# Performance work log

Hardware: AMD Instinct MI355X
Metric: run time of the kernel (lower is better)

## Reference

```python
import jax, jax.numpy as jnp
import numpy as np

H = 64  # hidden_dim

def _rnn_layer(x, Wih, Whh, bih, bhh):
    # x: [B, T, D_in] -> hidden states [B, T, H]; PyTorch RNN tanh cell:
    # h_t = tanh(W_ih x_t + b_ih + W_hh h_{t-1} + b_hh)
    B = x.shape[0]
    xp = jnp.einsum('btd,hd->bth', x, Wih) + bih  # precompute input projection
    h0 = jnp.zeros((B, H), dtype=x.dtype)
    def step(h, xt):
        h = jnp.tanh(xt + h @ Whh.T + bhh)
        return h, h
    _, hs = jax.lax.scan(step, h0, jnp.swapaxes(xp, 0, 1))  # scan over T
    return jnp.swapaxes(hs, 0, 1)  # [B, T, H]

def setup_inputs() -> dict:
    key = jax.random.key(0)
    ks = jax.random.split(key, 14)
    B, T, D = 4096, 512, 1
    s = 0.1  # small init scale to keep tanh unsaturated
    inp = {
        'x': jax.random.normal(ks[0], (B, T, D), dtype=jnp.float32),
        'W_ih0': jax.random.normal(ks[1], (H, D), dtype=jnp.float32) * s,
        'W_hh0': jax.random.normal(ks[2], (H, H), dtype=jnp.float32) * s,
        'b_ih0': jax.random.normal(ks[3], (H,), dtype=jnp.float32) * s,
        'b_hh0': jax.random.normal(ks[4], (H,), dtype=jnp.float32) * s,
        'W_ih1': jax.random.normal(ks[5], (H, H), dtype=jnp.float32) * s,
        'W_hh1': jax.random.normal(ks[6], (H, H), dtype=jnp.float32) * s,
        'b_ih1': jax.random.normal(ks[7], (H,), dtype=jnp.float32) * s,
        'b_hh1': jax.random.normal(ks[8], (H,), dtype=jnp.float32) * s,
        'fc1_W': jax.random.normal(ks[9], (64, H), dtype=jnp.float32) * s,
        'fc1_b': jax.random.normal(ks[10], (64,), dtype=jnp.float32) * s,
        'fc2_W': jax.random.normal(ks[11], (1, 64), dtype=jnp.float32) * s,
        'fc2_b': jax.random.normal(ks[12], (1,), dtype=jnp.float32) * s,
    }
    return inp

def reference(x, W_ih0, W_hh0, b_ih0, b_hh0, W_ih1, W_hh1, b_ih1, b_hh1,
              fc1_W, fc1_b, fc2_W, fc2_b):
    h1 = _rnn_layer(x, W_ih0, W_hh0, b_ih0, b_hh0)   # layer 0
    h2 = _rnn_layer(h1, W_ih1, W_hh1, b_ih1, b_hh1)  # layer 1
    last = h2[:, -1, :]                               # [B, H]
    z = jax.nn.relu(last @ fc1_W.T + fc1_b)
    return z @ fc2_W.T + fc2_b                        # [B, 1]
```

## Files before the change

kernel.cpp:

```cpp
#include <hip/hip_runtime.h>

namespace {

constexpr int T_LEN = 512;
constexpr int XS    = 516;

typedef _Float16 half8  __attribute__((ext_vector_type(8)));
typedef float    f32x4v __attribute__((ext_vector_type(4)));
typedef unsigned uint2v __attribute__((ext_vector_type(2)));
typedef unsigned uint4v __attribute__((ext_vector_type(4)));

#define MFMA16(a, b, c) __builtin_amdgcn_mfma_f32_16x16x32_f16((a), (b), (c), 0, 0, 0)

__device__ __forceinline__ half8 load_frag(const float* __restrict__ W,
                                           int row, int k0, float s) {
    const float* p = W + row * 64 + k0;
    f32x4v lo = *reinterpret_cast<const f32x4v*>(p);
    f32x4v hi = *reinterpret_cast<const f32x4v*>(p + 4);
    uint4v u;
    u.x = __builtin_bit_cast(unsigned, __builtin_amdgcn_cvt_pkrtz(lo.x * s, lo.y * s));
    u.y = __builtin_bit_cast(unsigned, __builtin_amdgcn_cvt_pkrtz(lo.z * s, lo.w * s));
    u.z = __builtin_bit_cast(unsigned, __builtin_amdgcn_cvt_pkrtz(hi.x * s, hi.y * s));
    u.w = __builtin_bit_cast(unsigned, __builtin_amdgcn_cvt_pkrtz(hi.z * s, hi.w * s));
    return __builtin_bit_cast(half8, u);
}

__device__ __forceinline__ void tanh4(f32x4v &a) {
#pragma unroll
    for (int q = 0; q < 4; ++q) {
        float e = __expf(a[q]);
        a[q] = 1.0f - 2.0f * __builtin_amdgcn_rcpf(e + 1.0f);
    }
}

__global__ __launch_bounds__(256, 2)
void rnn_mfma4_kernel(const float* __restrict__ x,
                      const float* __restrict__ Wih0,
                      const float* __restrict__ Whh0,
                      const float* __restrict__ bih0,
                      const float* __restrict__ bhh0,
                      const float* __restrict__ Wih1,
                      const float* __restrict__ Whh1,
                      const float* __restrict__ bih1,
                      const float* __restrict__ bhh1,
                      const float* __restrict__ fc1W,
                      const float* __restrict__ fc1b,
                      const float* __restrict__ fc2W,
                      const float* __restrict__ fc2b,
                      float* __restrict__ out)
{
    const int tid    = threadIdx.x;
    const int wv     = tid >> 6;
    const int lane   = tid & 63;
    const int g      = lane >> 4;
    const int b16    = lane & 15;
    const int batch0 = blockIdx.x * 16;

    __shared__ float    sx[16 * XS];
    __shared__ _Float16 sh1[2][16][72];
    __shared__ _Float16 sh2[2][16][72];
    __shared__ float    pf[4][16];

    {
        const float* gx = x + (size_t)batch0 * T_LEN;
#pragma unroll
        for (int c = 0; c < 8; ++c) {
            int idx = tid + c * 256;
            int r = idx >> 7, c4 = idx & 127;
            f32x4v v = *reinterpret_cast<const f32x4v*>(gx + r * T_LEN + c4 * 4);
            *reinterpret_cast<f32x4v*>(&sx[r * XS + c4 * 4]) = v;
        }
    }

    const int row = 16 * wv + b16;
    const half8 WA0_0 = load_frag(Whh0, row,      8 * g, 2.0f);
    const half8 WA0_1 = load_frag(Whh0, row, 32 + 8 * g, 2.0f);
    const half8 WI1_0 = load_frag(Wih1, row,      8 * g, 2.0f);
    const half8 WI1_1 = load_frag(Wih1, row, 32 + 8 * g, 2.0f);
    const half8 WH1_0 = load_frag(Whh1, row,      8 * g, 2.0f);
    const half8 WH1_1 = load_frag(Whh1, row, 32 + 8 * g, 2.0f);

    f32x4v bb0, bb1, wx2;
#pragma unroll
    for (int q = 0; q < 4; ++q) {
        const int o = 16 * wv + 4 * g + q;
        bb0[q] = 2.0f * (bih0[o] + bhh0[o]);
        bb1[q] = 2.0f * (bih1[o] + bhh1[o]);
        wx2[q] = 2.0f * Wih0[o];
    }
    const int o2 = 16 * wv + 4 * g;

    auto publish = [&](_Float16* base, const f32x4v& a) {
        uint2v p;
        p.x = __builtin_bit_cast(unsigned, __builtin_amdgcn_cvt_pkrtz(a[0], a[1]));
        p.y = __builtin_bit_cast(unsigned, __builtin_amdgcn_cvt_pkrtz(a[2], a[3]));
        *reinterpret_cast<uint2v*>(base + b16 * 72 + o2) = p;
    };
    auto rdfrag = [&](const _Float16* base, int k0) -> half8 {
        return *reinterpret_cast<const half8*>(base + b16 * 72 + k0);
    };

    half8 Bh1_0, Bh1_1, Bh2_0, Bh2_1;

    __syncthreads();

    float xt = sx[b16 * XS + 0];
    float xn = sx[b16 * XS + 1];

    {
        f32x4v a0 = wx2 * xt + bb0;
        tanh4(a0);
        publish(&sh1[0][0][0], a0);
        *reinterpret_cast<uint2v*>(&sh2[0][0][0] + b16 * 72 + o2) = uint2v{0, 0};
        __syncthreads();
        Bh1_0 = rdfrag(&sh1[0][0][0],      8 * g);
        Bh1_1 = rdfrag(&sh1[0][0][0], 32 + 8 * g);
        Bh2_0 = rdfrag(&sh2[0][0][0],      8 * g);
        Bh2_1 = rdfrag(&sh2[0][0][0], 32 + 8 * g);
        xt = xn; xn = sx[b16 * XS + 2];
    }

#pragma unroll 2
    for (int k = 1; k < T_LEN; ++k) {
        const int s = k & 1;
        const float xf = sx[b16 * XS + k + 2];

        f32x4v a0 = wx2 * xt + bb0;
        a0 = MFMA16(WA0_0, Bh1_0, a0);
        a0 = MFMA16(WA0_1, Bh1_1, a0);

        f32x4v zz = {};
        f32x4v u  = MFMA16(WI1_0, Bh1_0, bb1);
        u  = MFMA16(WI1_1, Bh1_1, u);
        f32x4v v4 = MFMA16(WH1_0, Bh2_0, zz);
        v4 = MFMA16(WH1_1, Bh2_1, v4);
        f32x4v a1 = u + v4;

        tanh4(a0);
        tanh4(a1);
        publish(&sh1[s][0][0], a0);
        publish(&sh2[s][0][0], a1);
        __syncthreads();
        Bh1_0 = rdfrag(&sh1[s][0][0],      8 * g);
        Bh1_1 = rdfrag(&sh1[s][0][0], 32 + 8 * g);
        Bh2_0 = rdfrag(&sh2[s][0][0],      8 * g);
        Bh2_1 = rdfrag(&sh2[s][0][0], 32 + 8 * g);
        xt = xn; xn = xf;
    }

    {
        f32x4v zz = {};
        f32x4v u  = MFMA16(WI1_0, Bh1_0, bb1);
        u  = MFMA16(WI1_1, Bh1_1, u);
        f32x4v v4 = MFMA16(WH1_0, Bh2_0, zz);
        v4 = MFMA16(WH1_1, Bh2_1, v4);
        f32x4v a1 = u + v4;
        tanh4(a1);
        publish(&sh2[0][0][0], a1);
        __syncthreads();
        Bh2_0 = rdfrag(&sh2[0][0][0],      8 * g);
        Bh2_1 = rdfrag(&sh2[0][0][0], 32 + 8 * g);
    }

    const half8 F0 = load_frag(fc1W, row,      8 * g, 1.0f);
    const half8 F1 = load_frag(fc1W, row, 32 + 8 * g, 1.0f);
    f32x4v zf;
#pragma unroll
    for (int q = 0; q < 4; ++q) zf[q] = fc1b[16 * wv + 4 * g + q];
    zf = MFMA16(F0, Bh2_0, zf);
    zf = MFMA16(F1, Bh2_1, zf);

    float pacc = 0.0f;
#pragma unroll
    for (int q = 0; q < 4; ++q)
        pacc += fmaxf(zf[q], 0.0f) * fc2W[16 * wv + 4 * g + q];
    pacc += __shfl_xor(pacc, 16);
    pacc += __shfl_xor(pacc, 32);
    if (lane < 16) pf[wv][lane] = pacc;
    __syncthreads();
    if (tid < 16)
        out[batch0 + tid] = pf[0][tid] + pf[1][tid] + pf[2][tid] + pf[3][tid]
                          + fc2b[0];
}

}

extern "C" void kernel_launch(void* const* d_in, const int* in_sizes, int n_in,
                              void* d_out, int out_size, void* d_ws, size_t ws_size,
                              hipStream_t stream) {
    (void)n_in; (void)out_size; (void)d_ws; (void)ws_size;
    const float* x    = (const float*)d_in[0];
    const float* Wih0 = (const float*)d_in[1];
    const float* Whh0 = (const float*)d_in[2];
    const float* bih0 = (const float*)d_in[3];
    const float* bhh0 = (const float*)d_in[4];
    const float* Wih1 = (const float*)d_in[5];
    const float* Whh1 = (const float*)d_in[6];
    const float* bih1 = (const float*)d_in[7];
    const float* bhh1 = (const float*)d_in[8];
    const float* fc1W = (const float*)d_in[9];
    const float* fc1b = (const float*)d_in[10];
    const float* fc2W = (const float*)d_in[11];
    const float* fc2b = (const float*)d_in[12];
    float* out = (float*)d_out;

    const int B = in_sizes[0] / T_LEN;
    dim3 grid(B / 16), block(256);
    rnn_mfma4_kernel<<<grid, block, 0, stream>>>(
        x, Wih0, Whh0, bih0, bhh0, Wih1, Whh1, bih1, bhh1,
        fc1W, fc1b, fc2W, fc2b, out);
}
```

Measured before the change: 143.7 us.

## Split recurrent matmuls into K=16 MFMAs and precompute own-slice contribution before barrier

Switches from 16x16x32 to 16x16x16 f16 MFMAs so each wave's recurrent matmul splits into per-16-column chunks. The chunk from the wave's own freshly computed hidden slice is accumulated in registers before the barrier, taking it off the critical path after each sync. Only the three other waves' slices are read from LDS, which now uses a swizzled layout to avoid bank conflicts. This issues more, smaller MFMAs and more LDS reads per step, and lowers launch bounds to one block per SIMD, which may cut occupancy.

```diff
diff --git a/kernel.cpp b/kernel.cpp
--- a/kernel.cpp
+++ b/kernel.cpp
@@ -5,24 +5,23 @@
 constexpr int T_LEN = 512;
 constexpr int XS    = 516;
 
-typedef _Float16 half8  __attribute__((ext_vector_type(8)));
+typedef _Float16 half4  __attribute__((ext_vector_type(4)));
 typedef float    f32x4v __attribute__((ext_vector_type(4)));
 typedef unsigned uint2v __attribute__((ext_vector_type(2)));
-typedef unsigned uint4v __attribute__((ext_vector_type(4)));
-
-#define MFMA16(a, b, c) __builtin_amdgcn_mfma_f32_16x16x32_f16((a), (b), (c), 0, 0, 0)
-
-__device__ __forceinline__ half8 load_frag(const float* __restrict__ W,
-                                           int row, int k0, float s) {
-    const float* p = W + row * 64 + k0;
-    f32x4v lo = *reinterpret_cast<const f32x4v*>(p);
-    f32x4v hi = *reinterpret_cast<const f32x4v*>(p + 4);
-    uint4v u;
-    u.x = __builtin_bit_cast(unsigned, __builtin_amdgcn_cvt_pkrtz(lo.x * s, lo.y * s));
-    u.y = __builtin_bit_cast(unsigned, __builtin_amdgcn_cvt_pkrtz(lo.z * s, lo.w * s));
-    u.z = __builtin_bit_cast(unsigned, __builtin_amdgcn_cvt_pkrtz(hi.x * s, hi.y * s));
-    u.w = __builtin_bit_cast(unsigned, __builtin_amdgcn_cvt_pkrtz(hi.z * s, hi.w * s));
-    return __builtin_bit_cast(half8, u);
+
+#define MFMA16(a, b, c) __builtin_amdgcn_mfma_f32_16x16x16f16((a), (b), (c), 0, 0, 0)
+
+__device__ __forceinline__ half4 cvt_h4(f32x4v a) {
+    uint2v u;
+    u.x = __builtin_bit_cast(unsigned, __builtin_amdgcn_cvt_pkrtz(a[0], a[1]));
+    u.y = __builtin_bit_cast(unsigned, __builtin_amdgcn_cvt_pkrtz(a[2], a[3]));
+    return __builtin_bit_cast(half4, u);
+}
+
+__device__ __forceinline__ half4 load_q(const float* __restrict__ W,
+                                        int row, int k0, float s) {
+    f32x4v v = *reinterpret_cast<const f32x4v*>(W + row * 64 + k0);
+    return cvt_h4(v * s);
 }
 
 __device__ __forceinline__ void tanh4(f32x4v &a) {
@@ -33,21 +32,32 @@
     }
 }
 
-__global__ __launch_bounds__(256, 2)
-void rnn_mfma4_kernel(const float* __restrict__ x,
-                      const float* __restrict__ Wih0,
-                      const float* __restrict__ Whh0,
-                      const float* __restrict__ bih0,
-                      const float* __restrict__ bhh0,
-                      const float* __restrict__ Wih1,
-                      const float* __restrict__ Whh1,
-                      const float* __restrict__ bih1,
-                      const float* __restrict__ bhh1,
-                      const float* __restrict__ fc1W,
-                      const float* __restrict__ fc1b,
-                      const float* __restrict__ fc2W,
-                      const float* __restrict__ fc2b,
-                      float* __restrict__ out)
+__device__ __forceinline__ _Float16* swzp(_Float16* base, int b, int r0) {
+    int d = (b << 5) + (r0 >> 1);
+    d ^= (b & 7) << 2;
+    return base + (d << 1);
+}
+__device__ __forceinline__ const _Float16* swzc(const _Float16* base, int b, int r0) {
+    int d = (b << 5) + (r0 >> 1);
+    d ^= (b & 7) << 2;
+    return base + (d << 1);
+}
+
+__global__ __launch_bounds__(256, 1)
+void rnn_k16_kernel(const float* __restrict__ x,
+                    const float* __restrict__ Wih0,
+                    const float* __restrict__ Whh0,
+                    const float* __restrict__ bih0,
+                    const float* __restrict__ bhh0,
+                    const float* __restrict__ Wih1,
+                    const float* __restrict__ Whh1,
+                    const float* __restrict__ bih1,
+                    const float* __restrict__ bhh1,
+                    const float* __restrict__ fc1W,
+                    const float* __restrict__ fc1b,
+                    const float* __restrict__ fc2W,
+                    const float* __restrict__ fc2b,
+                    float* __restrict__ out)
 {
     const int tid    = threadIdx.x;
     const int wv     = tid >> 6;
@@ -57,8 +67,8 @@
     const int batch0 = blockIdx.x * 16;
 
     __shared__ float    sx[16 * XS];
-    __shared__ _Float16 sh1[2][16][72];
-    __shared__ _Float16 sh2[2][16][72];
+    __shared__ _Float16 sh1[2][16 * 64];
+    __shared__ _Float16 sh2[2][16 * 64];
     __shared__ float    pf[4][16];
 
     {
@@ -73,12 +83,20 @@
     }
 
     const int row = 16 * wv + b16;
-    const half8 WA0_0 = load_frag(Whh0, row,      8 * g, 2.0f);
-    const half8 WA0_1 = load_frag(Whh0, row, 32 + 8 * g, 2.0f);
-    const half8 WI1_0 = load_frag(Wih1, row,      8 * g, 2.0f);
-    const half8 WI1_1 = load_frag(Wih1, row, 32 + 8 * g, 2.0f);
-    const half8 WH1_0 = load_frag(Whh1, row,      8 * g, 2.0f);
-    const half8 WH1_1 = load_frag(Whh1, row, 32 + 8 * g, 2.0f);
+    const int q0 = (wv + 1) & 3, q1 = (wv + 2) & 3, q2 = (wv + 3) & 3;
+
+    const half4 A0own = load_q(Whh0, row, 16 * wv + 4 * g, 2.0f);
+    const half4 A0o0  = load_q(Whh0, row, 16 * q0 + 4 * g, 2.0f);
+    const half4 A0o1  = load_q(Whh0, row, 16 * q1 + 4 * g, 2.0f);
+    const half4 A0o2  = load_q(Whh0, row, 16 * q2 + 4 * g, 2.0f);
+    const half4 I1own = load_q(Wih1, row, 16 * wv + 4 * g, 2.0f);
+    const half4 I1o0  = load_q(Wih1, row, 16 * q0 + 4 * g, 2.0f);
+    const half4 I1o1  = load_q(Wih1, row, 16 * q1 + 4 * g, 2.0f);
+    const half4 I1o2  = load_q(Wih1, row, 16 * q2 + 4 * g, 2.0f);
+    const half4 H1own = load_q(Whh1, row, 16 * wv + 4 * g, 2.0f);
+    const half4 H1o0  = load_q(Whh1, row, 16 * q0 + 4 * g, 2.0f);
+    const half4 H1o1  = load_q(Whh1, row, 16 * q1 + 4 * g, 2.0f);
+    const half4 H1o2  = load_q(Whh1, row, 16 * q2 + 4 * g, 2.0f);
 
     f32x4v bb0, bb1, wx2;
 #pragma unroll
@@ -88,95 +106,119 @@
         bb1[q] = 2.0f * (bih1[o] + bhh1[o]);
         wx2[q] = 2.0f * Wih0[o];
     }
-    const int o2 = 16 * wv + 4 * g;
-
-    auto publish = [&](_Float16* base, const f32x4v& a) {
-        uint2v p;
-        p.x = __builtin_bit_cast(unsigned, __builtin_amdgcn_cvt_pkrtz(a[0], a[1]));
-        p.y = __builtin_bit_cast(unsigned, __builtin_amdgcn_cvt_pkrtz(a[2], a[3]));
-        *reinterpret_cast<uint2v*>(base + b16 * 72 + o2) = p;
-    };
-    auto rdfrag = [&](const _Float16* base, int k0) -> half8 {
-        return *reinterpret_cast<const half8*>(base + b16 * 72 + k0);
-    };
-
-    half8 Bh1_0, Bh1_1, Bh2_0, Bh2_1;
+    const int ro = 16 * wv + 4 * g;
 
     __syncthreads();
 
-    float xt = sx[b16 * XS + 0];
-    float xn = sx[b16 * XS + 1];
-
-    {
-        f32x4v a0 = wx2 * xt + bb0;
+    f32x4v p0, p1;
+    {
+        const float x0 = sx[b16 * XS + 0];
+        const float x1 = sx[b16 * XS + 1];
+        f32x4v a0 = wx2 * x0 + bb0;
         tanh4(a0);
-        publish(&sh1[0][0][0], a0);
-        *reinterpret_cast<uint2v*>(&sh2[0][0][0] + b16 * 72 + o2) = uint2v{0, 0};
+        half4 b1own = cvt_h4(a0);
+        *reinterpret_cast<half4*>(swzp(sh1[0], b16, ro)) = b1own;
+        half4 z4 = {};
+        *reinterpret_cast<half4*>(swzp(sh2[0], b16, ro)) = z4;
+        p0 = MFMA16(A0own, b1own, wx2 * x1 + bb0);
+        p1 = MFMA16(I1own, b1own, bb1);
         __syncthreads();
-        Bh1_0 = rdfrag(&sh1[0][0][0],      8 * g);
-        Bh1_1 = rdfrag(&sh1[0][0][0], 32 + 8 * g);
-        Bh2_0 = rdfrag(&sh2[0][0][0],      8 * g);
-        Bh2_1 = rdfrag(&sh2[0][0][0], 32 + 8 * g);
-        xt = xn; xn = sx[b16 * XS + 2];
     }
 
 #pragma unroll 2
     for (int k = 1; k < T_LEN; ++k) {
-        const int s = k & 1;
-        const float xf = sx[b16 * XS + k + 2];
-
-        f32x4v a0 = wx2 * xt + bb0;
-        a0 = MFMA16(WA0_0, Bh1_0, a0);
-        a0 = MFMA16(WA0_1, Bh1_1, a0);
+        const int s  = k & 1;
+        const int rd = s ^ 1;
+        const _Float16* r1 = sh1[rd];
+        const _Float16* r2 = sh2[rd];
+
+        half4 f10 = *reinterpret_cast<const half4*>(swzc(r1, b16, 16 * q0 + 4 * g));
+        half4 f11 = *reinterpret_cast<const half4*>(swzc(r1, b16, 16 * q1 + 4 * g));
+        half4 f12 = *reinterpret_cast<const half4*>(swzc(r1, b16, 16 * q2 + 4 * g));
+        half4 f20 = *reinterpret_cast<const half4*>(swzc(r2, b16, 16 * q0 + 4 * g));
+        half4 f21 = *reinterpret_cast<const half4*>(swzc(r2, b16, 16 * q1 + 4 * g));
+        half4 f22 = *reinterpret_cast<const half4*>(swzc(r2, b16, 16 * q2 + 4 * g));
+        const float xk1 = sx[b16 * XS + k + 1];
 
         f32x4v zz = {};
-        f32x4v u  = MFMA16(WI1_0, Bh1_0, bb1);
-        u  = MFMA16(WI1_1, Bh1_1, u);
-        f32x4v v4 = MFMA16(WH1_0, Bh2_0, zz);
-        v4 = MFMA16(WH1_1, Bh2_1, v4);
-        f32x4v a1 = u + v4;
-
+        f32x4v u  = MFMA16(A0o0, f10, p0);
+        f32x4v v  = MFMA16(A0o1, f11, zz);
+        u = MFMA16(A0o2, f12, u);
+        f32x4v a0 = u + v;
         tanh4(a0);
+        half4 b1own = cvt_h4(a0);
+        *reinterpret_cast<half4*>(swzp(sh1[s], b16, ro)) = b1own;
+
+        f32x4v u1 = MFMA16(I1o0, f10, p1);
+        f32x4v v1 = MFMA16(I1o1, f11, zz);
+        u1 = MFMA16(I1o2, f12, u1);
+        v1 = MFMA16(H1o0, f20, v1);
+        u1 = MFMA16(H1o1, f21, u1);
+        v1 = MFMA16(H1o2, f22, v1);
+        f32x4v a1 = u1 + v1;
         tanh4(a1);
-        publish(&sh1[s][0][0], a0);
-        publish(&sh2[s][0][0], a1);
+        half4 b2own = cvt_h4(a1);
+        *reinterpret_cast<half4*>(swzp(sh2[s], b16, ro)) = b2own;
+
+        p0 = MFMA16(A0own, b1own, wx2 * xk1 + bb0);
+        p1 = MFMA16(I1own, b1own, bb1);
+        p1 = MFMA16(H1own, b2own, p1);
+
         __syncthreads();
-        Bh1_0 = rdfrag(&sh1[s][0][0],      8 * g);
-        Bh1_1 = rdfrag(&sh1[s][0][0], 32 + 8 * g);
-        Bh2_0 = rdfrag(&sh2[s][0][0],      8 * g);
-        Bh2_1 = rdfrag(&sh2[s][0][0], 32 + 8 * g);
-        xt = xn; xn = xf;
-    }
-
-    {
+    }
+
+    half4 b2fin;
+    {
+        const _Float16* r1 = sh1[1];
+        const _Float16* r2 = sh2[1];
+        half4 f10 = *reinterpret_cast<const half4*>(swzc(r1, b16, 16 * q0 + 4 * g));
+        half4 f11 = *reinterpret_cast<const half4*>(swzc(r1, b16, 16 * q1 + 4 * g));
+        half4 f12 = *reinterpret_cast<const half4*>(swzc(r1, b16, 16 * q2 + 4 * g));
+        half4 f20 = *reinterpret_cast<const half4*>(swzc(r2, b16, 16 * q0 + 4 * g));
+        half4 f21 = *reinterpret_cast<const half4*>(swzc(r2, b16, 16 * q1 + 4 * g));
+        half4 f22 = *reinterpret_cast<const half4*>(swzc(r2, b16, 16 * q2 + 4 * g));
         f32x4v zz = {};
-        f32x4v u  = MFMA16(WI1_0, Bh1_0, bb1);
-        u  = MFMA16(WI1_1, Bh1_1, u);
-        f32x4v v4 = MFMA16(WH1_0, Bh2_0, zz);
-        v4 = MFMA16(WH1_1, Bh2_1, v4);
-        f32x4v a1 = u + v4;
+        f32x4v u1 = MFMA16(I1o0, f10, p1);
+        f32x4v v1 = MFMA16(I1o1, f11, zz);
+        u1 = MFMA16(I1o2, f12, u1);
+        v1 = MFMA16(H1o0, f20, v1);
+        u1 = MFMA16(H1o1, f21, u1);
+        v1 = MFMA16(H1o2, f22, v1);
+        f32x4v a1 = u1 + v1;
         tanh4(a1);
-        publish(&sh2[0][0][0], a1);
+        b2fin = cvt_h4(a1);
+        *reinterpret_cast<half4*>(swzp(sh2[0], b16, ro)) = b2fin;
         __syncthreads();
-        Bh2_0 = rdfrag(&sh2[0][0][0],      8 * g);
-        Bh2_1 = rdfrag(&sh2[0][0][0], 32 + 8 * g);
-    }
-
-    const half8 F0 = load_frag(fc1W, row,      8 * g, 1.0f);
-    const half8 F1 = load_frag(fc1W, row, 32 + 8 * g, 1.0f);
-    f32x4v zf;
-#pragma unroll
-    for (int q = 0; q < 4; ++q) zf[q] = fc1b[16 * wv + 4 * g + q];
-    zf = MFMA16(F0, Bh2_0, zf);
-    zf = MFMA16(F1, Bh2_1, zf);
-
-    float pacc = 0.0f;
-#pragma unroll
-    for (int q = 0; q < 4; ++q)
-        pacc += fmaxf(zf[q], 0.0f) * fc2W[16 * wv + 4 * g + q];
-    pacc += __shfl_xor(pacc, 16);
-    pacc += __shfl_xor(pacc, 32);
-    if (lane < 16) pf[wv][lane] = pacc;
+    }
+
+    {
+        const half4 Fown = load_q(fc1W, row, 16 * wv + 4 * g, 1.0f);
+        const half4 Fo0  = load_q(fc1W, row, 16 * q0 + 4 * g, 1.0f);
+        const half4 Fo1  = load_q(fc1W, row, 16 * q1 + 4 * g, 1.0f);
+        const half4 Fo2  = load_q(fc1W, row, 16 * q2 + 4 * g, 1.0f);
+        const _Float16* r2 = sh2[0];
+        half4 e0 = *reinterpret_cast<const half4*>(swzc(r2, b16, 16 * q0 + 4 * g));
+        half4 e1 = *reinterpret_cast<const half4*>(swzc(r2, b16, 16 * q1 + 4 * g));
+        half4 e2 = *reinterpret_cast<const half4*>(swzc(r2, b16, 16 * q2 + 4 * g));
+
+        f32x4v zb;
+#pragma unroll
+        for (int q = 0; q < 4; ++q) zb[q] = fc1b[16 * wv + 4 * g + q];
+        f32x4v zz = {};
+        f32x4v zu = MFMA16(Fown, b2fin, zb);
+        f32x4v zv = MFMA16(Fo0, e0, zz);
+        zu = MFMA16(Fo1, e1, zu);
+        zv = MFMA16(Fo2, e2, zv);
+        f32x4v zf = zu + zv;
+
+        float pacc = 0.0f;
+#pragma unroll
+        for (int q = 0; q < 4; ++q)
+            pacc += fmaxf(zf[q], 0.0f) * fc2W[16 * wv + 4 * g + q];
+        pacc += __shfl_xor(pacc, 16);
+        pacc += __shfl_xor(pacc, 32);
+        if (lane < 16) pf[wv][lane] = pacc;
+    }
     __syncthreads();
     if (tid < 16)
         out[batch0 + tid] = pf[0][tid] + pf[1][tid] + pf[2][tid] + pf[3][tid]
@@ -206,7 +248,7 @@
 
     const int B = in_sizes[0] / T_LEN;
     dim3 grid(B / 16), block(256);
-    rnn_mfma4_kernel<<<grid, block, 0, stream>>>(
+    rnn_k16_kernel<<<grid, block, 0, stream>>>(
         x, Wih0, Whh0, bih0, bhh0, Wih1, Whh1, bih1, bhh1,
         fc1W, fc1b, fc2W, fc2b, out);
 }
```

Result: slower. 169.3 us (+17.9%).

## Split RNN layers across two wave groups per block for wavefront pipelining

Applied to the files above, without the earlier changes.

Doubles the block to 512 threads and gives layer 0 to waves 0-3 and layer 1 to waves 4-7. The two layers run as a skewed pipeline: layer 1 at step t consumes layer 0's output from step t-1 through double-buffered shared memory, with one barrier per step. This halves the serial MFMA and tanh work per wave on the critical path, but the 512-thread barrier now spans eight waves, the load is uneven (layer 1 does twice the MFMAs), and doubling threads per block may reduce how many blocks fit per CU.

```diff
diff --git a/kernel.cpp b/kernel.cpp
--- a/kernel.cpp
+++ b/kernel.cpp
@@ -5,12 +5,13 @@
 constexpr int T_LEN = 512;
 constexpr int XS    = 516;
 
+typedef _Float16 half4  __attribute__((ext_vector_type(4)));
 typedef _Float16 half8  __attribute__((ext_vector_type(8)));
 typedef float    f32x4v __attribute__((ext_vector_type(4)));
 typedef unsigned uint2v __attribute__((ext_vector_type(2)));
 typedef unsigned uint4v __attribute__((ext_vector_type(4)));
 
-#define MFMA16(a, b, c) __builtin_amdgcn_mfma_f32_16x16x32_f16((a), (b), (c), 0, 0, 0)
+#define MFMA32(a, b, c) __builtin_amdgcn_mfma_f32_16x16x32_f16((a), (b), (c), 0, 0, 0)
 
 __device__ __forceinline__ half8 load_frag(const float* __restrict__ W,
                                            int row, int k0, float s) {
@@ -33,8 +34,8 @@
     }
 }
 
-__global__ __launch_bounds__(256, 2)
-void rnn_mfma4_kernel(const float* __restrict__ x,
+__global__ __launch_bounds__(512, 2)
+void rnn_split_kernel(const float* __restrict__ x,
                       const float* __restrict__ Wih0,
                       const float* __restrict__ Whh0,
                       const float* __restrict__ bih0,
@@ -50,22 +51,24 @@
                       float* __restrict__ out)
 {
     const int tid    = threadIdx.x;
-    const int wv     = tid >> 6;
+    const int wave   = tid >> 6;
+    const int grp    = wave >> 2;
+    const int wv     = wave & 3;
     const int lane   = tid & 63;
     const int g      = lane >> 4;
     const int b16    = lane & 15;
     const int batch0 = blockIdx.x * 16;
 
     __shared__ float    sx[16 * XS];
-    __shared__ _Float16 sh1[2][16][72];
-    __shared__ _Float16 sh2[2][16][72];
+    __shared__ _Float16 sh1[2][16 * 72];
+    __shared__ _Float16 sh2[2][16 * 72];
     __shared__ float    pf[4][16];
 
     {
         const float* gx = x + (size_t)batch0 * T_LEN;
 #pragma unroll
-        for (int c = 0; c < 8; ++c) {
-            int idx = tid + c * 256;
+        for (int c = 0; c < 4; ++c) {
+            int idx = tid + c * 512;
             int r = idx >> 7, c4 = idx & 127;
             f32x4v v = *reinterpret_cast<const f32x4v*>(gx + r * T_LEN + c4 * 4);
             *reinterpret_cast<f32x4v*>(&sx[r * XS + c4 * 4]) = v;
@@ -73,110 +76,106 @@
     }
 
     const int row = 16 * wv + b16;
-    const half8 WA0_0 = load_frag(Whh0, row,      8 * g, 2.0f);
-    const half8 WA0_1 = load_frag(Whh0, row, 32 + 8 * g, 2.0f);
-    const half8 WI1_0 = load_frag(Wih1, row,      8 * g, 2.0f);
-    const half8 WI1_1 = load_frag(Wih1, row, 32 + 8 * g, 2.0f);
-    const half8 WH1_0 = load_frag(Whh1, row,      8 * g, 2.0f);
-    const half8 WH1_1 = load_frag(Whh1, row, 32 + 8 * g, 2.0f);
-
-    f32x4v bb0, bb1, wx2;
-#pragma unroll
-    for (int q = 0; q < 4; ++q) {
-        const int o = 16 * wv + 4 * g + q;
-        bb0[q] = 2.0f * (bih0[o] + bhh0[o]);
-        bb1[q] = 2.0f * (bih1[o] + bhh1[o]);
-        wx2[q] = 2.0f * Wih0[o];
-    }
-    const int o2 = 16 * wv + 4 * g;
+    const int ro  = 16 * wv + 4 * g;
+
+    half8 WA0_0 = {}, WA0_1 = {};
+    half8 WI1_0 = {}, WI1_1 = {}, WH1_0 = {}, WH1_1 = {};
+    f32x4v bb0 = {}, wx2 = {}, bb1 = {};
+
+    if (grp == 0) {
+        WA0_0 = load_frag(Whh0, row,      8 * g, 2.0f);
+        WA0_1 = load_frag(Whh0, row, 32 + 8 * g, 2.0f);
+#pragma unroll
+        for (int q = 0; q < 4; ++q) {
+            const int o = 16 * wv + 4 * g + q;
+            bb0[q] = 2.0f * (bih0[o] + bhh0[o]);
+            wx2[q] = 2.0f * Wih0[o];
+        }
+    } else {
+        WI1_0 = load_frag(Wih1, row,      8 * g, 2.0f);
+        WI1_1 = load_frag(Wih1, row, 32 + 8 * g, 2.0f);
+        WH1_0 = load_frag(Whh1, row,      8 * g, 2.0f);
+        WH1_1 = load_frag(Whh1, row, 32 + 8 * g, 2.0f);
+#pragma unroll
+        for (int q = 0; q < 4; ++q) {
+            const int o = 16 * wv + 4 * g + q;
+            bb1[q] = 2.0f * (bih1[o] + bhh1[o]);
+        }
+    }
 
     auto publish = [&](_Float16* base, const f32x4v& a) {
         uint2v p;
         p.x = __builtin_bit_cast(unsigned, __builtin_amdgcn_cvt_pkrtz(a[0], a[1]));
         p.y = __builtin_bit_cast(unsigned, __builtin_amdgcn_cvt_pkrtz(a[2], a[3]));
-        *reinterpret_cast<uint2v*>(base + b16 * 72 + o2) = p;
+        *reinterpret_cast<uint2v*>(base + b16 * 72 + ro) = p;
     };
     auto rdfrag = [&](const _Float16* base, int k0) -> half8 {
         return *reinterpret_cast<const half8*>(base + b16 * 72 + k0);
     };
 
-    half8 Bh1_0, Bh1_1, Bh2_0, Bh2_1;
-
+    if (grp == 0) {
+        *reinterpret_cast<uint2v*>(&sh1[1][0] + b16 * 72 + ro) = uint2v{0, 0};
+        const float x0 = sx[b16 * XS + 0];
+        f32x4v a0 = wx2 * x0 + bb0;
+        tanh4(a0);
+        publish(sh1[0], a0);
+    } else {
+        *reinterpret_cast<uint2v*>(&sh2[0][0] + b16 * 72 + ro) = uint2v{0, 0};
+    }
     __syncthreads();
 
-    float xt = sx[b16 * XS + 0];
-    float xn = sx[b16 * XS + 1];
-
-    {
-        f32x4v a0 = wx2 * xt + bb0;
-        tanh4(a0);
-        publish(&sh1[0][0][0], a0);
-        *reinterpret_cast<uint2v*>(&sh2[0][0][0] + b16 * 72 + o2) = uint2v{0, 0};
+#pragma unroll 2
+    for (int t = 1; t <= T_LEN; ++t) {
+        const int s = t & 1;
+        const int r = s ^ 1;
+        if (grp == 0) {
+            if (t < T_LEN) {
+                half8 B0 = rdfrag(sh1[r],      8 * g);
+                half8 B1 = rdfrag(sh1[r], 32 + 8 * g);
+                const float xt = sx[b16 * XS + t];
+                f32x4v a0 = wx2 * xt + bb0;
+                a0 = MFMA32(WA0_0, B0, a0);
+                a0 = MFMA32(WA0_1, B1, a0);
+                tanh4(a0);
+                publish(sh1[s], a0);
+            }
+        } else {
+            half8 B10 = rdfrag(sh1[r],      8 * g);
+            half8 B11 = rdfrag(sh1[r], 32 + 8 * g);
+            half8 B20 = rdfrag(sh2[r],      8 * g);
+            half8 B21 = rdfrag(sh2[r], 32 + 8 * g);
+            f32x4v zz = {};
+            f32x4v u = MFMA32(WI1_0, B10, bb1);
+            u = MFMA32(WI1_1, B11, u);
+            f32x4v v = MFMA32(WH1_0, B20, zz);
+            v = MFMA32(WH1_1, B21, v);
+            f32x4v a1 = u + v;
+            tanh4(a1);
+            publish(sh2[s], a1);
+        }
         __syncthreads();
-        Bh1_0 = rdfrag(&sh1[0][0][0],      8 * g);
-        Bh1_1 = rdfrag(&sh1[0][0][0], 32 + 8 * g);
-        Bh2_0 = rdfrag(&sh2[0][0][0],      8 * g);
-        Bh2_1 = rdfrag(&sh2[0][0][0], 32 + 8 * g);
-        xt = xn; xn = sx[b16 * XS + 2];
-    }
-
-#pragma unroll 2
-    for (int k = 1; k < T_LEN; ++k) {
-        const int s = k & 1;
-        const float xf = sx[b16 * XS + k + 2];
-
-        f32x4v a0 = wx2 * xt + bb0;
-        a0 = MFMA16(WA0_0, Bh1_0, a0);
-        a0 = MFMA16(WA0_1, Bh1_1, a0);
-
-        f32x4v zz = {};
-        f32x4v u  = MFMA16(WI1_0, Bh1_0, bb1);
-        u  = MFMA16(WI1_1, Bh1_1, u);
-        f32x4v v4 = MFMA16(WH1_0, Bh2_0, zz);
-        v4 = MFMA16(WH1_1, Bh2_1, v4);
-        f32x4v a1 = u + v4;
-
-        tanh4(a0);
-        tanh4(a1);
-        publish(&sh1[s][0][0], a0);
-        publish(&sh2[s][0][0], a1);
-        __syncthreads();
-        Bh1_0 = rdfrag(&sh1[s][0][0],      8 * g);
-        Bh1_1 = rdfrag(&sh1[s][0][0], 32 + 8 * g);
-        Bh2_0 = rdfrag(&sh2[s][0][0],      8 * g);
-        Bh2_1 = rdfrag(&sh2[s][0][0], 32 + 8 * g);
-        xt = xn; xn = xf;
-    }
-
-    {
-        f32x4v zz = {};
-        f32x4v u  = MFMA16(WI1_0, Bh1_0, bb1);
-        u  = MFMA16(WI1_1, Bh1_1, u);
-        f32x4v v4 = MFMA16(WH1_0, Bh2_0, zz);
-        v4 = MFMA16(WH1_1, Bh2_1, v4);
-        f32x4v a1 = u + v4;
-        tanh4(a1);
-        publish(&sh2[0][0][0], a1);
-        __syncthreads();
-        Bh2_0 = rdfrag(&sh2[0][0][0],      8 * g);
-        Bh2_1 = rdfrag(&sh2[0][0][0], 32 + 8 * g);
-    }
-
-    const half8 F0 = load_frag(fc1W, row,      8 * g, 1.0f);
-    const half8 F1 = load_frag(fc1W, row, 32 + 8 * g, 1.0f);
-    f32x4v zf;
-#pragma unroll
-    for (int q = 0; q < 4; ++q) zf[q] = fc1b[16 * wv + 4 * g + q];
-    zf = MFMA16(F0, Bh2_0, zf);
-    zf = MFMA16(F1, Bh2_1, zf);
-
-    float pacc = 0.0f;
-#pragma unroll
-    for (int q = 0; q < 4; ++q)
-        pacc += fmaxf(zf[q], 0.0f) * fc2W[16 * wv + 4 * g + q];
-    pacc += __shfl_xor(pacc, 16);
-    pacc += __shfl_xor(pacc, 32);
-    if (lane < 16) pf[wv][lane] = pacc;
+    }
+
+
+    if (grp == 0) {
+        const half8 F0 = load_frag(fc1W, row,      8 * g, 1.0f);
+        const half8 F1 = load_frag(fc1W, row, 32 + 8 * g, 1.0f);
+        half8 E0 = rdfrag(sh2[0],      8 * g);
+        half8 E1 = rdfrag(sh2[0], 32 + 8 * g);
+        f32x4v zf;
+#pragma unroll
+        for (int q = 0; q < 4; ++q) zf[q] = fc1b[16 * wv + 4 * g + q];
+        zf = MFMA32(F0, E0, zf);
+        zf = MFMA32(F1, E1, zf);
+
+        float pacc = 0.0f;
+#pragma unroll
+        for (int q = 0; q < 4; ++q)
+            pacc += fmaxf(zf[q], 0.0f) * fc2W[16 * wv + 4 * g + q];
+        pacc += __shfl_xor(pacc, 16);
+        pacc += __shfl_xor(pacc, 32);
+        if (lane < 16) pf[wv][lane] = pacc;
+    }
     __syncthreads();
     if (tid < 16)
         out[batch0 + tid] = pf[0][tid] + pf[1][tid] + pf[2][tid] + pf[3][tid]
@@ -205,8 +204,8 @@
     float* out = (float*)d_out;
 
     const int B = in_sizes[0] / T_LEN;
-    dim3 grid(B / 16), block(256);
-    rnn_mfma4_kernel<<<grid, block, 0, stream>>>(
+    dim3 grid(B / 16), block(512);
+    rnn_split_kernel<<<grid, block, 0, stream>>>(
         x, Wih0, Whh0, bih0, bhh0, Wih1, Whh1, bih1, bhh1,
         fc1W, fc1b, fc2W, fc2b, out);
 }
```

After: 181.2 us. 26.1% more time.

## Halve batch tile to 8 per block, use exp2 tanh, split MFMA chains

Applied to the files above, without the earlier changes.

Each block now handles 8 batch rows instead of 16, doubling the grid to 512 blocks so more CUs get work. The 16-wide MFMA columns are still computed but duplicated, with lanes 8-15 mirroring rows 0-7. The tanh uses a base-2 scale folded into the weights so exp2 replaces expf. The two K-halves of each recurrent MFMA are split into independent accumulators to shorten the dependency chain. Half the MFMA work per block is now redundant, so total compute doubles in exchange for lower per-block latency.

```diff
diff --git a/kernel.cpp b/kernel.cpp
--- a/kernel.cpp
+++ b/kernel.cpp
@@ -4,13 +4,24 @@
 
 constexpr int T_LEN = 512;
 constexpr int XS    = 516;
+constexpr int TILE  = 8;
 
 typedef _Float16 half8  __attribute__((ext_vector_type(8)));
 typedef float    f32x4v __attribute__((ext_vector_type(4)));
 typedef unsigned uint2v __attribute__((ext_vector_type(2)));
 typedef unsigned uint4v __attribute__((ext_vector_type(4)));
 
-#define MFMA16(a, b, c) __builtin_amdgcn_mfma_f32_16x16x32_f16((a), (b), (c), 0, 0, 0)
+#define MFMA32(a, b, c) __builtin_amdgcn_mfma_f32_16x16x32_f16((a), (b), (c), 0, 0, 0)
+
+constexpr float SCL = 2.8853900817779268f;
+
+__device__ __forceinline__ float exp2_fast(float x) {
+#if __has_builtin(__builtin_amdgcn_exp2f)
+    return __builtin_amdgcn_exp2f(x);
+#else
+    return exp2f(x);
+#endif
+}
 
 __device__ __forceinline__ half8 load_frag(const float* __restrict__ W,
                                            int row, int k0, float s) {
@@ -28,43 +39,44 @@
 __device__ __forceinline__ void tanh4(f32x4v &a) {
 #pragma unroll
     for (int q = 0; q < 4; ++q) {
-        float e = __expf(a[q]);
+        float e = exp2_fast(a[q]);
         a[q] = 1.0f - 2.0f * __builtin_amdgcn_rcpf(e + 1.0f);
     }
 }
 
 __global__ __launch_bounds__(256, 2)
-void rnn_mfma4_kernel(const float* __restrict__ x,
-                      const float* __restrict__ Wih0,
-                      const float* __restrict__ Whh0,
-                      const float* __restrict__ bih0,
-                      const float* __restrict__ bhh0,
-                      const float* __restrict__ Wih1,
-                      const float* __restrict__ Whh1,
-                      const float* __restrict__ bih1,
-                      const float* __restrict__ bhh1,
-                      const float* __restrict__ fc1W,
-                      const float* __restrict__ fc1b,
-                      const float* __restrict__ fc2W,
-                      const float* __restrict__ fc2b,
-                      float* __restrict__ out)
+void rnn_b8_kernel(const float* __restrict__ x,
+                   const float* __restrict__ Wih0,
+                   const float* __restrict__ Whh0,
+                   const float* __restrict__ bih0,
+                   const float* __restrict__ bhh0,
+                   const float* __restrict__ Wih1,
+                   const float* __restrict__ Whh1,
+                   const float* __restrict__ bih1,
+                   const float* __restrict__ bhh1,
+                   const float* __restrict__ fc1W,
+                   const float* __restrict__ fc1b,
+                   const float* __restrict__ fc2W,
+                   const float* __restrict__ fc2b,
+                   float* __restrict__ out)
 {
     const int tid    = threadIdx.x;
     const int wv     = tid >> 6;
     const int lane   = tid & 63;
     const int g      = lane >> 4;
     const int b16    = lane & 15;
-    const int batch0 = blockIdx.x * 16;
-
-    __shared__ float    sx[16 * XS];
-    __shared__ _Float16 sh1[2][16][72];
-    __shared__ _Float16 sh2[2][16][72];
+    const int bb     = b16 & (TILE - 1);
+    const int batch0 = blockIdx.x * TILE;
+
+    __shared__ float    sx[TILE * XS];
+    __shared__ _Float16 sh1[2][16 * 72];
+    __shared__ _Float16 sh2[2][16 * 72];
     __shared__ float    pf[4][16];
 
     {
         const float* gx = x + (size_t)batch0 * T_LEN;
 #pragma unroll
-        for (int c = 0; c < 8; ++c) {
+        for (int c = 0; c < TILE * T_LEN / 4 / 256; ++c) {
             int idx = tid + c * 256;
             int r = idx >> 7, c4 = idx & 127;
             f32x4v v = *reinterpret_cast<const f32x4v*>(gx + r * T_LEN + c4 * 4);
@@ -73,28 +85,29 @@
     }
 
     const int row = 16 * wv + b16;
-    const half8 WA0_0 = load_frag(Whh0, row,      8 * g, 2.0f);
-    const half8 WA0_1 = load_frag(Whh0, row, 32 + 8 * g, 2.0f);
-    const half8 WI1_0 = load_frag(Wih1, row,      8 * g, 2.0f);
-    const half8 WI1_1 = load_frag(Wih1, row, 32 + 8 * g, 2.0f);
-    const half8 WH1_0 = load_frag(Whh1, row,      8 * g, 2.0f);
-    const half8 WH1_1 = load_frag(Whh1, row, 32 + 8 * g, 2.0f);
+    const int ro  = 16 * wv + 4 * g;
+
+    const half8 WA0_0 = load_frag(Whh0, row,      8 * g, SCL);
+    const half8 WA0_1 = load_frag(Whh0, row, 32 + 8 * g, SCL);
+    const half8 WI1_0 = load_frag(Wih1, row,      8 * g, SCL);
+    const half8 WI1_1 = load_frag(Wih1, row, 32 + 8 * g, SCL);
+    const half8 WH1_0 = load_frag(Whh1, row,      8 * g, SCL);
+    const half8 WH1_1 = load_frag(Whh1, row, 32 + 8 * g, SCL);
 
     f32x4v bb0, bb1, wx2;
 #pragma unroll
     for (int q = 0; q < 4; ++q) {
         const int o = 16 * wv + 4 * g + q;
-        bb0[q] = 2.0f * (bih0[o] + bhh0[o]);
-        bb1[q] = 2.0f * (bih1[o] + bhh1[o]);
-        wx2[q] = 2.0f * Wih0[o];
-    }
-    const int o2 = 16 * wv + 4 * g;
+        bb0[q] = SCL * (bih0[o] + bhh0[o]);
+        bb1[q] = SCL * (bih1[o] + bhh1[o]);
+        wx2[q] = SCL * Wih0[o];
+    }
 
     auto publish = [&](_Float16* base, const f32x4v& a) {
         uint2v p;
         p.x = __builtin_bit_cast(unsigned, __builtin_amdgcn_cvt_pkrtz(a[0], a[1]));
         p.y = __builtin_bit_cast(unsigned, __builtin_amdgcn_cvt_pkrtz(a[2], a[3]));
-        *reinterpret_cast<uint2v*>(base + b16 * 72 + o2) = p;
+        *reinterpret_cast<uint2v*>(base + b16 * 72 + ro) = p;
     };
     auto rdfrag = [&](const _Float16* base, int k0) -> half8 {
         return *reinterpret_cast<const half8*>(base + b16 * 72 + k0);
@@ -104,81 +117,84 @@
 
     __syncthreads();
 
-    float xt = sx[b16 * XS + 0];
-    float xn = sx[b16 * XS + 1];
+    float xt = sx[bb * XS + 0];
+    float xn = sx[bb * XS + 1];
 
     {
         f32x4v a0 = wx2 * xt + bb0;
         tanh4(a0);
-        publish(&sh1[0][0][0], a0);
-        *reinterpret_cast<uint2v*>(&sh2[0][0][0] + b16 * 72 + o2) = uint2v{0, 0};
+        publish(sh1[0], a0);
+        *reinterpret_cast<uint2v*>(&sh2[0][0] + b16 * 72 + ro) = uint2v{0, 0};
         __syncthreads();
-        Bh1_0 = rdfrag(&sh1[0][0][0],      8 * g);
-        Bh1_1 = rdfrag(&sh1[0][0][0], 32 + 8 * g);
-        Bh2_0 = rdfrag(&sh2[0][0][0],      8 * g);
-        Bh2_1 = rdfrag(&sh2[0][0][0], 32 + 8 * g);
-        xt = xn; xn = sx[b16 * XS + 2];
+        Bh1_0 = rdfrag(sh1[0],      8 * g);
+        Bh1_1 = rdfrag(sh1[0], 32 + 8 * g);
+        Bh2_0 = rdfrag(sh2[0],      8 * g);
+        Bh2_1 = rdfrag(sh2[0], 32 + 8 * g);
+        xt = xn; xn = sx[bb * XS + 2];
     }
 
 #pragma unroll 2
     for (int k = 1; k < T_LEN; ++k) {
         const int s = k & 1;
-        const float xf = sx[b16 * XS + k + 2];
-
-        f32x4v a0 = wx2 * xt + bb0;
-        a0 = MFMA16(WA0_0, Bh1_0, a0);
-        a0 = MFMA16(WA0_1, Bh1_1, a0);
+        const float xf = sx[bb * XS + k + 2];
 
         f32x4v zz = {};
-        f32x4v u  = MFMA16(WI1_0, Bh1_0, bb1);
-        u  = MFMA16(WI1_1, Bh1_1, u);
-        f32x4v v4 = MFMA16(WH1_0, Bh2_0, zz);
-        v4 = MFMA16(WH1_1, Bh2_1, v4);
-        f32x4v a1 = u + v4;
-
+        f32x4v u0 = MFMA32(WA0_0, Bh1_0, wx2 * xt + bb0);
+        f32x4v v0 = MFMA32(WA0_1, Bh1_1, zz);
+        f32x4v u1 = MFMA32(WI1_0, Bh1_0, bb1);
+        f32x4v v1 = MFMA32(WH1_0, Bh2_0, zz);
+        u1 = MFMA32(WI1_1, Bh1_1, u1);
+        v1 = MFMA32(WH1_1, Bh2_1, v1);
+
+        f32x4v a0 = u0 + v0;
         tanh4(a0);
+        publish(sh1[s], a0);
+
+        f32x4v a1 = u1 + v1;
         tanh4(a1);
-        publish(&sh1[s][0][0], a0);
-        publish(&sh2[s][0][0], a1);
+        publish(sh2[s], a1);
+
         __syncthreads();
-        Bh1_0 = rdfrag(&sh1[s][0][0],      8 * g);
-        Bh1_1 = rdfrag(&sh1[s][0][0], 32 + 8 * g);
-        Bh2_0 = rdfrag(&sh2[s][0][0],      8 * g);
-        Bh2_1 = rdfrag(&sh2[s][0][0], 32 + 8 * g);
+        Bh1_0 = rdfrag(sh1[s],      8 * g);
+        Bh1_1 = rdfrag(sh1[s], 32 + 8 * g);
+        Bh2_0 = rdfrag(sh2[s],      8 * g);
+        Bh2_1 = rdfrag(sh2[s], 32 + 8 * g);
         xt = xn; xn = xf;
     }
 
     {
         f32x4v zz = {};
-        f32x4v u  = MFMA16(WI1_0, Bh1_0, bb1);
-        u  = MFMA16(WI1_1, Bh1_1, u);
-        f32x4v v4 = MFMA16(WH1_0, Bh2_0, zz);
-        v4 = MFMA16(WH1_1, Bh2_1, v4);
-        f32x4v a1 = u + v4;
+        f32x4v u1 = MFMA32(WI1_0, Bh1_0, bb1);
+        f32x4v v1 = MFMA32(WH1_0, Bh2_0, zz);
+        u1 = MFMA32(WI1_1, Bh1_1, u1);
+        v1 = MFMA32(WH1_1, Bh2_1, v1);
+        f32x4v a1 = u1 + v1;
         tanh4(a1);
-        publish(&sh2[0][0][0], a1);
+        publish(sh2[0], a1);
         __syncthreads();
-        Bh2_0 = rdfrag(&sh2[0][0][0],      8 * g);
-        Bh2_1 = rdfrag(&sh2[0][0][0], 32 + 8 * g);
-    }
-
-    const half8 F0 = load_frag(fc1W, row,      8 * g, 1.0f);
-    const half8 F1 = load_frag(fc1W, row, 32 + 8 * g, 1.0f);
-    f32x4v zf;
-#pragma unroll
-    for (int q = 0; q < 4; ++q) zf[q] = fc1b[16 * wv + 4 * g + q];
-    zf = MFMA16(F0, Bh2_0, zf);
-    zf = MFMA16(F1, Bh2_1, zf);
-
-    float pacc = 0.0f;
-#pragma unroll
-    for (int q = 0; q < 4; ++q)
-        pacc += fmaxf(zf[q], 0.0f) * fc2W[16 * wv + 4 * g + q];
-    pacc += __shfl_xor(pacc, 16);
-    pacc += __shfl_xor(pacc, 32);
-    if (lane < 16) pf[wv][lane] = pacc;
+        Bh2_0 = rdfrag(sh2[0],      8 * g);
+        Bh2_1 = rdfrag(sh2[0], 32 + 8 * g);
+    }
+
+    {
+        const half8 F0 = load_frag(fc1W, row,      8 * g, 1.0f);
+        const half8 F1 = load_frag(fc1W, row, 32 + 8 * g, 1.0f);
+        f32x4v zf;
+#pragma unroll
+        for (int q = 0; q < 4; ++q) zf[q] = fc1b[16 * wv + 4 * g + q];
+        zf = MFMA32(F0, Bh2_0, zf);
+        zf = MFMA32(F1, Bh2_1, zf);
+
+        float pacc = 0.0f;
+#pragma unroll
+        for (int q = 0; q < 4; ++q)
+            pacc += fmaxf(zf[q], 0.0f) * fc2W[16 * wv + 4 * g + q];
+        pacc += __shfl_xor(pacc, 16);
+        pacc += __shfl_xor(pacc, 32);
+        if (lane < 16) pf[wv][lane] = pacc;
+    }
     __syncthreads();
-    if (tid < 16)
+    if (tid < TILE)
         out[batch0 + tid] = pf[0][tid] + pf[1][tid] + pf[2][tid] + pf[3][tid]
                           + fc2b[0];
 }
@@ -205,8 +221,8 @@
     float* out = (float*)d_out;
 
     const int B = in_sizes[0] / T_LEN;
-    dim3 grid(B / 16), block(256);
-    rnn_mfma4_kernel<<<grid, block, 0, stream>>>(
+    dim3 grid(B / TILE), block(256);
+    rnn_b8_kernel<<<grid, block, 0, stream>>>(
         x, Wih0, Whh0, bih0, bhh0, Wih1, Whh1, bih1, bhh1,
         fc1W, fc1b, fc2W, fc2b, out);
 }
```

Result: slower. 201.5 us (+40.3%).
